# Kernel optimization log

Hardware: AMD Instinct MI355X
Metric: run time of the kernel (lower is better)

The kernel has to match this reference:

```python
import jax, jax.numpy as jnp
import numpy as np

C = 64
HW = 21 * 21  # 441
NEIGHBOR_K = 3


def setup_inputs() -> dict:
    key = jax.random.key(0)
    k1, k2, k3, k4 = jax.random.split(key, 4)
    B1, B2 = 32, 25
    x1 = jax.random.normal(k1, (B1, C, 21, 21), dtype=jnp.float32)
    x2 = jax.random.normal(k2, (B2, C, 21, 21), dtype=jnp.float32)
    mask1 = jax.random.uniform(k3, (B1, 21, 21), dtype=jnp.float32)
    mask2 = jax.random.uniform(k4, (B2, 21, 21), dtype=jnp.float32)
    return {"x1": x1, "x2": x2, "mask1": mask1, "mask2": mask2}


def reference(x1, x2, mask1, mask2):
    B1 = x1.shape[0]
    B2 = x2.shape[0]
    q = x1.reshape(B1, C, HW)  # (B1, 64, 441) query descriptors
    s = x2.reshape(B2, C, HW)  # (B2, 64, 441) support descriptors
    # per-descriptor L2 norms over channel dim
    qn = jnp.linalg.norm(q, axis=1)  # (B1, 441)
    sn = jnp.linalg.norm(s, axis=1)  # (B2, 441)
    # cosine similarity between every query descriptor and every support descriptor
    inner = jnp.einsum('aci,bcj->abij', q, s)  # (B1, B2, 441, 441)
    sim = inner / (qn[:, None, :, None] * sn[None, :, None, :])
    # mask out invalid spatial positions on both sides
    sim = sim * mask1.reshape(B1, 1, HW, 1) * mask2.reshape(1, B2, 1, HW)
    # top-k nearest support descriptors per query descriptor, sum over all
    topk_vals, _ = jax.lax.top_k(sim, NEIGHBOR_K)  # (B1, B2, 441, k)
    return topk_vals.reshape(B1, B2, -1).sum(axis=2)  # (B1, B2)
```

## Files before the change

### kernel.cpp

```cpp
#include <hip/hip_runtime.h>
#include <math.h>

#define CCH 64
#define HW 441
#define HWP 448
#define NT 28
#define NB2 25
#define PANEL (HWP * CCH)

typedef _Float16 half8 __attribute__((ext_vector_type(8)));
typedef __fp16 h2 __attribute__((ext_vector_type(2)));
typedef float f32x4 __attribute__((ext_vector_type(4)));

__global__ __launch_bounds__(64) void normalize_frag_kernel(
        const float* __restrict__ x1, const float* __restrict__ m1,
        const float* __restrict__ x2, const float* __restrict__ m2,
        _Float16* __restrict__ qh, _Float16* __restrict__ sh,
        float* __restrict__ out, int nout, int n1rows, int nrows) {
    int idx = blockIdx.x * blockDim.x + threadIdx.x;
    if (idx < nout) out[idx] = 0.f;
    if (idx >= nrows) return;
    const float* x; const float* mk; _Float16* outp; int rb;
    if (idx < n1rows) { x = x1; mk = m1; outp = qh; rb = idx; }
    else             { x = x2; mk = m2; outp = sh; rb = idx - n1rows; }
    int b = rb / HWP, i = rb - b * HWP;
    float vals[CCH];
    if (i < HW) {
        const float* xb = x + (size_t)b * CCH * HW + i;
        float ss = 0.f;
#pragma unroll
        for (int c = 0; c < CCH; ++c) { float v = xb[c * HW]; vals[c] = v; ss += v * v; }
        float scale = mk[b * HW + i] * rsqrtf(ss);
#pragma unroll
        for (int c = 0; c < CCH; ++c) vals[c] *= scale;
    } else {
#pragma unroll
        for (int c = 0; c < CCH; ++c) vals[c] = 0.f;
    }
    _Float16* pb = outp + (size_t)b * PANEL + (i >> 4) * 1024 + (i & 15) * 8;
#pragma unroll
    for (int f = 0; f < 2; ++f) {
#pragma unroll
        for (int qd = 0; qd < 4; ++qd) {
            half8 h;
#pragma unroll
            for (int e = 0; e < 8; ++e) h[e] = (_Float16)vals[f * 32 + qd * 8 + e];
            *(half8*)(pb + f * 512 + qd * 128) = h;
        }
    }
}

static __device__ __forceinline__ h2 hmax2(h2 a, h2 b) {
    return __builtin_elementwise_max(a, b);
}
static __device__ __forceinline__ h2 hmin2(h2 a, h2 b) {
    return __builtin_elementwise_min(a, b);
}

#define PK_INSERT(v, p0, p1, p2)           \
    do {                                   \
        h2 _m = hmax2(p0, v);              \
        h2 _c = hmin2(p0, v);              \
        p0 = _m;                           \
        _m = hmax2(p1, _c);                \
        _c = hmin2(p1, _c);                \
        p1 = _m;                           \
        p2 = hmax2(p2, _c);                \
    } while (0)

#define MERGE3(t0, t1, t2, b0, b1, b2)            \
    do {                                          \
        float _m0 = fmaxf(t0, b0);                \
        float _n0 = fminf(t0, b0);                \
        float _m1 = fmaxf(t1, b1);                \
        float _t2 = fmaxf(t2, b2);                \
        t0 = _m0;                                 \
        t1 = fmaxf(_n0, _m1);                     \
        t2 = fmaxf(fminf(_n0, _m1), _t2);         \
    } while (0)

template <int NI>
__device__ __forceinline__ float do_pass(const _Float16* __restrict__ qtiles,
                                         const _Float16* __restrict__ spanel,
                                         int lane, int quad) {
    const float NEG = -1e30f;
    const f32x4 FZ = {0.f, 0.f, 0.f, 0.f};
    const h2 NEGH = {(__fp16)-65504.f, (__fp16)-65504.f};
    half8 bf0[NI], bf1[NI];
#pragma unroll
    for (int t = 0; t < NI; ++t) {
        const _Float16* qp = qtiles + t * 1024 + lane * 8;
        bf0[t] = *(const half8*)qp;
        bf1[t] = *(const half8*)(qp + 512);
    }
    h2 p0[NI], p1[NI], p2[NI];
#pragma unroll
    for (int t = 0; t < NI; ++t) { p0[t] = NEGH; p1[t] = NEGH; p2[t] = NEGH; }

    const _Float16* sp = spanel + lane * 8;
    half8 c0 = *(const half8*)sp;
    half8 c1 = *(const half8*)(sp + 512);
    half8 n0 = *(const half8*)(sp + 1024);
    half8 n1 = *(const half8*)(sp + 1024 + 512);

    for (int jt = 0; jt < NT - 1; ++jt) {
        int pf = (jt + 2 < NT) ? jt + 2 : NT - 1;
        const _Float16* pp = sp + pf * 1024;
        half8 f0 = *(const half8*)pp;
        half8 f1 = *(const half8*)(pp + 512);
#pragma unroll
        for (int t = 0; t < NI; ++t) {
            f32x4 z = __builtin_amdgcn_mfma_f32_16x16x32_f16(c0, bf0[t], FZ, 0, 0, 0);
            z = __builtin_amdgcn_mfma_f32_16x16x32_f16(c1, bf1[t], z, 0, 0, 0);
            h2 c02 = __builtin_amdgcn_cvt_pkrtz(z[0], z[2]);
            h2 c13 = __builtin_amdgcn_cvt_pkrtz(z[1], z[3]);
            PK_INSERT(c02, p0[t], p1[t], p2[t]);
            PK_INSERT(c13, p0[t], p1[t], p2[t]);
        }
        c0 = n0; c1 = n1; n0 = f0; n1 = f1;
    }
    {
#pragma unroll
        for (int t = 0; t < NI; ++t) {
            f32x4 z = __builtin_amdgcn_mfma_f32_16x16x32_f16(c0, bf0[t], FZ, 0, 0, 0);
            z = __builtin_amdgcn_mfma_f32_16x16x32_f16(c1, bf1[t], z, 0, 0, 0);
#pragma unroll
            for (int r = 0; r < 4; ++r)
                if (quad * 4 + r >= 9) z[r] = NEG;
            h2 c02 = __builtin_amdgcn_cvt_pkrtz(z[0], z[2]);
            h2 c13 = __builtin_amdgcn_cvt_pkrtz(z[1], z[3]);
            PK_INSERT(c02, p0[t], p1[t], p2[t]);
            PK_INSERT(c13, p0[t], p1[t], p2[t]);
        }
    }

    float res = 0.f;
#pragma unroll
    for (int t = 0; t < NI; ++t) {
        float t0 = (float)p0[t][0], t1 = (float)p1[t][0], t2 = (float)p2[t][0];
        float b0 = (float)p0[t][1], b1 = (float)p1[t][1], b2 = (float)p2[t][1];
        MERGE3(t0, t1, t2, b0, b1, b2);
        b0 = __shfl_xor(t0, 16); b1 = __shfl_xor(t1, 16); b2 = __shfl_xor(t2, 16);
        MERGE3(t0, t1, t2, b0, b1, b2);
        b0 = __shfl_xor(t0, 32); b1 = __shfl_xor(t1, 32); b2 = __shfl_xor(t2, 32);
        MERGE3(t0, t1, t2, b0, b1, b2);
        res += t0 + t1 + t2;
    }
    return (quad == 0) ? res : 0.f;
}

__global__ __launch_bounds__(128, 4) void sim_topk_mfma(const _Float16* __restrict__ qh,
                                                        const _Float16* __restrict__ sh,
                                                        float* __restrict__ out) {
    int blk = blockIdx.x;
    int pair = blk >> 1, g = blk & 1;
    int a = pair / NB2, b = pair - a * NB2;
    int tid = threadIdx.x, wave = tid >> 6, lane = tid & 63, quad = lane >> 4;
    int group = g * 2 + wave;
    const _Float16* qtiles = qh + (size_t)a * PANEL + (size_t)group * 7 * 1024;
    const _Float16* spanel = sh + (size_t)b * PANEL;

    float wacc = do_pass<7>(qtiles, spanel, lane, quad);

#pragma unroll
    for (int off = 32; off > 0; off >>= 1) wacc += __shfl_down(wacc, off);
    if (lane == 0) atomicAdd(&out[pair], wacc);
}

extern "C" void kernel_launch(void* const* d_in, const int* in_sizes, int n_in,
                              void* d_out, int out_size, void* d_ws, size_t ws_size,
                              hipStream_t stream) {
    const float* x1 = (const float*)d_in[0];
    const float* x2 = (const float*)d_in[1];
    const float* m1 = (const float*)d_in[2];
    const float* m2 = (const float*)d_in[3];
    float* out = (float*)d_out;

    int B1 = in_sizes[0] / (CCH * HW);
    int B2 = in_sizes[1] / (CCH * HW);

    _Float16* qh = (_Float16*)d_ws;
    _Float16* sh = qh + (size_t)B1 * PANEL;

    int n1 = B1 * HWP, ntot = (B1 + B2) * HWP;
    normalize_frag_kernel<<<(ntot + 63) / 64, 64, 0, stream>>>(
        x1, m1, x2, m2, qh, sh, out, B1 * B2, n1, ntot);
    sim_topk_mfma<<<B1 * B2 * 2, 128, 0, stream>>>(qh, sh, out);
}
```

Measured before the change: 99.94 us.

## Split support tiles across waves and merge top-3 through shared memory

Each block now handles 4 query tiles instead of 14 and the two waves split the support tiles (14 and 13) rather than the query tiles. Per-wave partial top-3 lists are merged through shared memory before the atomic add. The grid grows from 2 to 7 blocks per pair, which shortens each wave's serial loop and adds parallelism. In exchange it pays for a block sync, a shared-memory merge and more atomics, and prefetch depth drops from two tiles to one.

```diff
diff --git a/kernel.cpp b/kernel.cpp
--- a/kernel.cpp
+++ b/kernel.cpp
@@ -7,6 +7,7 @@
 #define NT 28
 #define NB2 25
 #define PANEL (HWP * CCH)
+#define NI 4
 
 typedef _Float16 half8 __attribute__((ext_vector_type(8)));
 typedef __fp16 h2 __attribute__((ext_vector_type(2)));
@@ -79,10 +80,11 @@
         t2 = fmaxf(fminf(_n0, _m1), _t2);         \
     } while (0)
 
-template <int NI>
-__device__ __forceinline__ float do_pass(const _Float16* __restrict__ qtiles,
-                                         const _Float16* __restrict__ spanel,
-                                         int lane, int quad) {
+template <bool MASKED>
+__device__ __forceinline__ void do_pass_j(const _Float16* __restrict__ qtiles,
+                                          const _Float16* __restrict__ spanel,
+                                          int jt0, int nfull, int lane, int quad,
+                                          float (&t0)[NI], float (&t1)[NI], float (&t2)[NI]) {
     const float NEG = -1e30f;
     const f32x4 FZ = {0.f, 0.f, 0.f, 0.f};
     const h2 NEGH = {(__fp16)-65504.f, (__fp16)-65504.f};
@@ -97,17 +99,15 @@
 #pragma unroll
     for (int t = 0; t < NI; ++t) { p0[t] = NEGH; p1[t] = NEGH; p2[t] = NEGH; }
 
-    const _Float16* sp = spanel + lane * 8;
+    const _Float16* sp = spanel + (size_t)jt0 * 1024 + lane * 8;
     half8 c0 = *(const half8*)sp;
     half8 c1 = *(const half8*)(sp + 512);
-    half8 n0 = *(const half8*)(sp + 1024);
-    half8 n1 = *(const half8*)(sp + 1024 + 512);
-
-    for (int jt = 0; jt < NT - 1; ++jt) {
-        int pf = (jt + 2 < NT) ? jt + 2 : NT - 1;
-        const _Float16* pp = sp + pf * 1024;
-        half8 f0 = *(const half8*)pp;
-        half8 f1 = *(const half8*)(pp + 512);
+
+    for (int jt = 0; jt < nfull; ++jt) {
+        int nx = (jt + 1 < nfull + (MASKED ? 1 : 0)) ? jt + 1 : jt;
+        const _Float16* np = sp + (size_t)nx * 1024;
+        half8 n0 = *(const half8*)np;
+        half8 n1 = *(const half8*)(np + 512);
 #pragma unroll
         for (int t = 0; t < NI; ++t) {
             f32x4 z = __builtin_amdgcn_mfma_f32_16x16x32_f16(c0, bf0[t], FZ, 0, 0, 0);
@@ -117,9 +117,9 @@
             PK_INSERT(c02, p0[t], p1[t], p2[t]);
             PK_INSERT(c13, p0[t], p1[t], p2[t]);
         }
-        c0 = n0; c1 = n1; n0 = f0; n1 = f1;
-    }
-    {
+        c0 = n0; c1 = n1;
+    }
+    if (MASKED) {
 #pragma unroll
         for (int t = 0; t < NI; ++t) {
             f32x4 z = __builtin_amdgcn_mfma_f32_16x16x32_f16(c0, bf0[t], FZ, 0, 0, 0);
@@ -134,37 +134,57 @@
         }
     }
 
-    float res = 0.f;
 #pragma unroll
     for (int t = 0; t < NI; ++t) {
-        float t0 = (float)p0[t][0], t1 = (float)p1[t][0], t2 = (float)p2[t][0];
+        float a0 = (float)p0[t][0], a1 = (float)p1[t][0], a2 = (float)p2[t][0];
         float b0 = (float)p0[t][1], b1 = (float)p1[t][1], b2 = (float)p2[t][1];
-        MERGE3(t0, t1, t2, b0, b1, b2);
-        b0 = __shfl_xor(t0, 16); b1 = __shfl_xor(t1, 16); b2 = __shfl_xor(t2, 16);
-        MERGE3(t0, t1, t2, b0, b1, b2);
-        b0 = __shfl_xor(t0, 32); b1 = __shfl_xor(t1, 32); b2 = __shfl_xor(t2, 32);
-        MERGE3(t0, t1, t2, b0, b1, b2);
-        res += t0 + t1 + t2;
-    }
-    return (quad == 0) ? res : 0.f;
+        MERGE3(a0, a1, a2, b0, b1, b2);
+        b0 = __shfl_xor(a0, 16); b1 = __shfl_xor(a1, 16); b2 = __shfl_xor(a2, 16);
+        MERGE3(a0, a1, a2, b0, b1, b2);
+        b0 = __shfl_xor(a0, 32); b1 = __shfl_xor(a1, 32); b2 = __shfl_xor(a2, 32);
+        MERGE3(a0, a1, a2, b0, b1, b2);
+        t0[t] = a0; t1[t] = a1; t2[t] = a2;
+    }
 }
 
 __global__ __launch_bounds__(128, 4) void sim_topk_mfma(const _Float16* __restrict__ qh,
                                                         const _Float16* __restrict__ sh,
                                                         float* __restrict__ out) {
+    __shared__ float s_tri[2][NI][16][3];
     int blk = blockIdx.x;
-    int pair = blk >> 1, g = blk & 1;
+    int pair = blk / 7, g = blk - pair * 7;
     int a = pair / NB2, b = pair - a * NB2;
-    int tid = threadIdx.x, wave = tid >> 6, lane = tid & 63, quad = lane >> 4;
-    int group = g * 2 + wave;
-    const _Float16* qtiles = qh + (size_t)a * PANEL + (size_t)group * 7 * 1024;
+    int tid = threadIdx.x, wave = tid >> 6, lane = tid & 63;
+    int m = lane & 15, quad = lane >> 4;
+    const _Float16* qtiles = qh + (size_t)a * PANEL + (size_t)g * NI * 1024;
     const _Float16* spanel = sh + (size_t)b * PANEL;
 
-    float wacc = do_pass<7>(qtiles, spanel, lane, quad);
-
-#pragma unroll
-    for (int off = 32; off > 0; off >>= 1) wacc += __shfl_down(wacc, off);
-    if (lane == 0) atomicAdd(&out[pair], wacc);
+    float t0[NI], t1[NI], t2[NI];
+    if (wave == 0)
+        do_pass_j<false>(qtiles, spanel, 0, 14, lane, quad, t0, t1, t2);
+    else
+        do_pass_j<true>(qtiles, spanel, 14, 13, lane, quad, t0, t1, t2);
+
+    if (quad == 0) {
+#pragma unroll
+        for (int t = 0; t < NI; ++t) {
+            s_tri[wave][t][m][0] = t0[t];
+            s_tri[wave][t][m][1] = t1[t];
+            s_tri[wave][t][m][2] = t2[t];
+        }
+    }
+    __syncthreads();
+
+    if (wave == 0) {
+        int t = quad;
+        float a0 = s_tri[0][t][m][0], a1 = s_tri[0][t][m][1], a2 = s_tri[0][t][m][2];
+        float b0 = s_tri[1][t][m][0], b1 = s_tri[1][t][m][1], b2 = s_tri[1][t][m][2];
+        MERGE3(a0, a1, a2, b0, b1, b2);
+        float r = a0 + a1 + a2;
+#pragma unroll
+        for (int off = 32; off > 0; off >>= 1) r += __shfl_down(r, off);
+        if (lane == 0) atomicAdd(&out[pair], r);
+    }
 }
 
 extern "C" void kernel_launch(void* const* d_in, const int* in_sizes, int n_in,
@@ -185,5 +205,5 @@
     int n1 = B1 * HWP, ntot = (B1 + B2) * HWP;
     normalize_frag_kernel<<<(ntot + 63) / 64, 64, 0, stream>>>(
         x1, m1, x2, m2, qh, sh, out, B1 * B2, n1, ntot);
-    sim_topk_mfma<<<B1 * B2 * 2, 128, 0, stream>>>(qh, sh, out);
-}
+    sim_topk_mfma<<<B1 * B2 * 7, 128, 0, stream>>>(qh, sh, out);
+}
```

Measured after the change: 99.16 us. About the same (-0.8%).
